# Kernel optimization log

Hardware: AMD Instinct MI355X
Metric: run time of the kernel (lower is better)

## Reference

```python
import jax, jax.numpy as jnp
import numpy as np

N, E = 50000, 800000
C, NT, ET, H, D = 128, 8, 16, 64, 4
TOTAL_IN = 2 * C + 2 * NT + ET  # 288
EPS = 1e-5


def setup_inputs() -> dict:
    key = jax.random.key(0)
    ks = jax.random.split(key, 10)
    x = jax.random.normal(ks[0], (N, C), dtype=jnp.float32)
    edge_index = jax.random.randint(ks[1], (2, E), 0, N, dtype=jnp.int64)
    edge_types = jax.random.randint(ks[2], (E,), 0, ET, dtype=jnp.int64)
    node_types = jax.random.randint(ks[3], (N,), 0, NT, dtype=jnp.int64)
    ln_w = jnp.ones((TOTAL_IN,), dtype=jnp.float32)
    ln_b = jnp.zeros((TOTAL_IN,), dtype=jnp.float32)
    W1 = jax.random.normal(ks[4], (TOTAL_IN, H), dtype=jnp.float32) * 0.05
    b1 = jnp.zeros((H,), dtype=jnp.float32)
    W2 = jax.random.normal(ks[5], (H, D * D), dtype=jnp.float32) * 0.05
    b2 = jnp.zeros((D * D,), dtype=jnp.float32)
    return {"x": x, "edge_index": edge_index, "edge_types": edge_types,
            "node_types": node_types, "ln_w": ln_w, "ln_b": ln_b,
            "W1": W1, "b1": b1, "W2": W2, "b2": b2}


def reference(x, edge_index, edge_types, node_types, ln_w, ln_b, W1, b1, W2, b2):
    row, col = edge_index[0], edge_index[1]
    # edge gathers of node features and one-hot type encodings
    nt_oh = jax.nn.one_hot(node_types, NT, dtype=x.dtype)   # [N, NT]
    et_oh = jax.nn.one_hot(edge_types, ET, dtype=x.dtype)   # [E, ET]
    h = jnp.concatenate([x[row], x[col], nt_oh[row], nt_oh[col], et_oh], axis=-1)  # [E, 288]
    # LayerNorm
    mu = jnp.mean(h, axis=-1, keepdims=True)
    var = jnp.mean(jnp.square(h - mu), axis=-1, keepdims=True)
    h = (h - mu) * jax.lax.rsqrt(var + EPS) * ln_w + ln_b
    # small MLP
    h = jax.nn.relu(h @ W1 + b1) @ W2 + b2          # [E, D*D]
    h = h.reshape(-1, D, D)
    att = jax.nn.softmax(h, axis=-1)                 # row-stochastic per edge
    return jnp.eye(D, dtype=h.dtype)[None] - att     # [E, D, D]
```

## Files before the change

kernel.cpp:

```cpp
#include <hip/hip_runtime.h>
#include <hip/hip_bf16.h>

#define NN 50000
#define NE 800000
#define C 128
#define HH 64
#define TIN 288
#define LN_EPS 1e-5f

typedef __attribute__((ext_vector_type(8))) short bf16x8;
typedef __attribute__((ext_vector_type(4))) float f32x4;

#define ETT_OFF 512
#define B1F_OFF 2560
#define B2F_OFF 35328
#define OHU_OFF 37376
#define OHV_OFF 38400
#define SQ_OFF 39424
#define U_OFF 439424
#define V_OFF 6839424

__device__ __forceinline__ short f2bf(float f) {
    __hip_bfloat16 h = __float2bfloat16(f);
    return __builtin_bit_cast(short, h);
}
__device__ __forceinline__ float bf2f(short s) {
    unsigned int u = ((unsigned int)(unsigned short)s) << 16;
    return __builtin_bit_cast(float, u);
}

__global__ void prep_weights(const float* __restrict__ ln_w,
                             const float* __restrict__ ln_b,
                             const float* __restrict__ W1,
                             const float* __restrict__ b1,
                             const float* __restrict__ W2,
                             float* __restrict__ ws) {
    int gid = blockIdx.x * 256 + threadIdx.x;
    if (blockIdx.x == 0 && threadIdx.x < 64) {
        int l = threadIdx.x;
        float s = 0.f, c = 0.f;
        for (int k = 0; k < TIN; ++k) {
            float w = W1[k * HH + l];
            s += ln_w[k] * w;
            c += ln_b[k] * w;
        }
        ws[l] = s;
        ws[64 + l] = c + b1[l];
    }
    short* B1 = (short*)((char*)ws + B1F_OFF);
    for (int idx = gid; idx < 16384; idx += 8192) {
        int j = idx & 7, l = (idx >> 3) & 63, cc = (idx >> 9) & 3, kt = idx >> 11;
        int g = l >> 4, m = l & 15;
        int k = 32 * kt + 8 * g + j, n = 16 * cc + m;
        B1[idx] = f2bf(ln_w[k] * W1[k * HH + n]);
    }
    short* B2 = (short*)((char*)ws + B2F_OFF);
    for (int idx = gid; idx < 1024; idx += 8192) {
        int j = idx & 7, l = (idx >> 3) & 63, kt = idx >> 9;
        int g = l >> 4, m = l & 15;
        int k = 32 * kt + 8 * g + j;
        B2[idx] = f2bf(W2[k * 16 + m]);
    }
    short* ohu = (short*)((char*)ws + OHU_OFF);
    short* ohv = (short*)((char*)ws + OHV_OFF);
    for (int idx = gid; idx < 512; idx += 8192) {
        int t = idx >> 6, j = idx & 63;
        ohu[idx] = f2bf(ln_w[256 + t] * W1[(256 + t) * HH + j]);
        ohv[idx] = f2bf(ln_w[264 + t] * W1[(264 + t) * HH + j]);
    }
    short* ett = (short*)((char*)ws + ETT_OFF);
    for (int idx = gid; idx < 1024; idx += 8192) {
        int et = idx >> 6, j = idx & 63;
        int unit = (j >> 3) ^ (et & 7);
        ett[et * 64 + unit * 8 + (j & 7)] = f2bf(ln_w[272 + et] * W1[(272 + et) * HH + j]);
    }
}

__global__ __launch_bounds__(512) void node_uv(const float* __restrict__ x,
                                               const int* __restrict__ ntype,
                                               float* __restrict__ ws) {
    __shared__ __align__(16) short lds_n[16384 + 8 * 1024];
    int tid = threadIdx.x;
    {
        const float4* src = (const float4*)((const char*)ws + B1F_OFF);
        float4* dst = (float4*)lds_n;
        for (int i = tid; i < 2048; i += 512) dst[i] = src[i];
    }
    __syncthreads();

    int wave = tid >> 6, lane = tid & 63, m = lane & 15, g = lane >> 4;
    int tile = blockIdx.x * 128 + wave * 16;
    int n = tile + m;
    int nc = n < NN ? n : NN - 1;

    float sum = 0.f, sq = 0.f;
    bf16x8 a[4];
#pragma unroll
    for (int kt = 0; kt < 4; ++kt) {
        const float* p = x + (size_t)nc * C + kt * 32 + g * 8;
        float4 p0 = *(const float4*)p;
        float4 p1 = *(const float4*)(p + 4);
        float vv[8] = {p0.x, p0.y, p0.z, p0.w, p1.x, p1.y, p1.z, p1.w};
#pragma unroll
        for (int j = 0; j < 8; ++j) {
            sum += vv[j];
            sq = fmaf(vv[j], vv[j], sq);
            a[kt][j] = f2bf(vv[j]);
        }
    }
    sum += __shfl_xor(sum, 16); sum += __shfl_xor(sum, 32);
    sq  += __shfl_xor(sq, 16);  sq  += __shfl_xor(sq, 32);
    if (g == 0 && n < NN)
        ((float2*)((char*)ws + SQ_OFF))[n] = make_float2(sum, sq);

    f32x4 au[4], av[4];
#pragma unroll
    for (int cc = 0; cc < 4; ++cc) { au[cc] = (f32x4){0,0,0,0}; av[cc] = (f32x4){0,0,0,0}; }
#pragma unroll
    for (int kt = 0; kt < 4; ++kt) {
        const bf16x8* Bu = (const bf16x8*)(lds_n + (kt * 4) * 512);
        const bf16x8* Bv = (const bf16x8*)(lds_n + ((kt + 4) * 4) * 512);
#pragma unroll
        for (int cc = 0; cc < 4; ++cc) {
            au[cc] = __builtin_amdgcn_mfma_f32_16x16x32_bf16(a[kt], Bu[cc * 64 + lane], au[cc], 0, 0, 0);
            av[cc] = __builtin_amdgcn_mfma_f32_16x16x32_bf16(a[kt], Bv[cc * 64 + lane], av[cc], 0, 0, 0);
        }
    }

    int ntv[4];
#pragma unroll
    for (int i = 0; i < 4; ++i) {
        int nn = tile + 4 * g + i;
        ntv[i] = ntype[nn < NN ? nn : NN - 1];
    }
    const unsigned short* ohu = (const unsigned short*)((const char*)ws + OHU_OFF);
    const unsigned short* ohv = (const unsigned short*)((const char*)ws + OHV_OFF);
    unsigned short* uT = (unsigned short*)((char*)ws + U_OFF);
    unsigned short* vT = (unsigned short*)((char*)ws + V_OFF);
    short* tb = lds_n + 16384 + wave * 1024;
    int nst = tile + m;

#pragma unroll
    for (int cc = 0; cc < 4; ++cc)
#pragma unroll
        for (int i = 0; i < 4; ++i) {
            float val = au[cc][i] + bf2f((short)ohu[ntv[i] * 64 + 16 * cc + m]);
            int r16 = 4 * g + i;
            tb[(r16 * 64 + 16 * cc + m) ^ ((r16 & 7) << 3)] = f2bf(val);
        }
    if (nst < NN) {
#pragma unroll
        for (int s2 = 0; s2 < 2; ++s2) {
            int idx = (m * 64 + 16 * g + 8 * s2) ^ ((m & 7) << 3);
            *(bf16x8*)(uT + (size_t)nst * 64 + 16 * g + 8 * s2) = *(const bf16x8*)(tb + idx);
        }
    }
#pragma unroll
    for (int cc = 0; cc < 4; ++cc)
#pragma unroll
        for (int i = 0; i < 4; ++i) {
            float val = av[cc][i] + bf2f((short)ohv[ntv[i] * 64 + 16 * cc + m]);
            int r16 = 4 * g + i;
            tb[(r16 * 64 + 16 * cc + m) ^ ((r16 & 7) << 3)] = f2bf(val);
        }
    if (nst < NN) {
#pragma unroll
        for (int s2 = 0; s2 < 2; ++s2) {
            int idx = (m * 64 + 16 * g + 8 * s2) ^ ((m & 7) << 3);
            *(bf16x8*)(vT + (size_t)nst * 64 + 16 * g + 8 * s2) = *(const bf16x8*)(tb + idx);
        }
    }
}

__global__ __launch_bounds__(512) void edge_kernel(
    const int* __restrict__ ei,
    const int* __restrict__ etype,
    const float* __restrict__ ws,
    const float* __restrict__ b2,
    float* __restrict__ out) {
    __shared__ __align__(16) short lds_e[2048];
    int tid = threadIdx.x;
    if (tid < 128)
        ((float4*)lds_e)[tid] = *(const float4*)((const char*)ws + B2F_OFF + tid * 16);
    else if (tid < 256)
        ((float4*)lds_e)[tid] = *(const float4*)((const char*)ws + ETT_OFF + (tid - 128) * 16);
    __syncthreads();

    int wave = tid >> 6, lane = tid & 63, m = lane & 15, g = lane >> 4;
    int tile = blockIdx.x * 128 + wave * 16;
    int e = tile + m;

    int row = ei[e];
    int col = ei[NE + e];
    int et = etype[e];

    const float2* SQ = (const float2*)((const char*)ws + SQ_OFF);
    float2 sqr = SQ[row], sqc = SQ[col];
    const unsigned short* uT = (const unsigned short*)((const char*)ws + U_OFF);
    const unsigned short* vT = (const unsigned short*)((const char*)ws + V_OFF);
    bf16x8 U0 = *(const bf16x8*)(uT + (size_t)row * 64 + 8 * g);
    bf16x8 U1 = *(const bf16x8*)(uT + (size_t)row * 64 + 32 + 8 * g);
    bf16x8 V0 = *(const bf16x8*)(vT + (size_t)col * 64 + 8 * g);
    bf16x8 V1 = *(const bf16x8*)(vT + (size_t)col * 64 + 32 + 8 * g);
    const short* ett = lds_e + 1024;
    bf16x8 T0 = *(const bf16x8*)(ett + et * 64 + ((g ^ (et & 7)) << 3));
    bf16x8 T1 = *(const bf16x8*)(ett + et * 64 + (((4 + g) ^ (et & 7)) << 3));

    float mu = (sqr.x + sqc.x + 3.0f) * (1.0f / TIN);
    float var = (sqr.y + sqc.y + 3.0f) * (1.0f / TIN) - mu * mu;
    float rstd = rsqrtf(var + LN_EPS);

    const float* sst = ws;
    const float* cct = ws + 64;
    bf16x8 af0, af1;
    {
        f32x4 sA = *(const f32x4*)(sst + 8 * g);
        f32x4 sB = *(const f32x4*)(sst + 8 * g + 4);
        f32x4 cA = *(const f32x4*)(cct + 8 * g);
        f32x4 cB = *(const f32x4*)(cct + 8 * g + 4);
#pragma unroll
        for (int j = 0; j < 8; ++j) {
            float t = bf2f(U0[j]) + bf2f(V0[j]) + bf2f(T0[j]);
            float sv = (j < 4) ? sA[j] : sB[j - 4];
            float cv = (j < 4) ? cA[j] : cB[j - 4];
            float h = rstd * (t - mu * sv) + cv;
            af0[j] = f2bf(fmaxf(h, 0.f));
        }
    }
    {
        f32x4 sA = *(const f32x4*)(sst + 32 + 8 * g);
        f32x4 sB = *(const f32x4*)(sst + 32 + 8 * g + 4);
        f32x4 cA = *(const f32x4*)(cct + 32 + 8 * g);
        f32x4 cB = *(const f32x4*)(cct + 32 + 8 * g + 4);
#pragma unroll
        for (int j = 0; j < 8; ++j) {
            float t = bf2f(U1[j]) + bf2f(V1[j]) + bf2f(T1[j]);
            float sv = (j < 4) ? sA[j] : sB[j - 4];
            float cv = (j < 4) ? cA[j] : cB[j - 4];
            float h = rstd * (t - mu * sv) + cv;
            af1[j] = f2bf(fmaxf(h, 0.f));
        }
    }

    const bf16x8* B2f = (const bf16x8*)lds_e;
    f32x4 o = {0.f, 0.f, 0.f, 0.f};
    o = __builtin_amdgcn_mfma_f32_16x16x32_bf16(af0, B2f[lane], o, 0, 0, 0);
    o = __builtin_amdgcn_mfma_f32_16x16x32_bf16(af1, B2f[64 + lane], o, 0, 0, 0);

    float b2v = b2[m];
    int r4 = m >> 2, c4 = m & 3;
    float diag = (c4 == r4) ? 1.0f : 0.0f;
#pragma unroll
    for (int i = 0; i < 4; ++i) {
        float v = o[i] + b2v;
        float mx = fmaxf(v, __shfl_xor(v, 1));
        mx = fmaxf(mx, __shfl_xor(mx, 2));
        float ev = __expf(v - mx);
        float sd = ev + __shfl_xor(ev, 1);
        sd += __shfl_xor(sd, 2);
        out[(size_t)(tile + 4 * g + i) * 16 + m] = diag - ev / sd;
    }
}

extern "C" void kernel_launch(void* const* d_in, const int* in_sizes, int n_in,
                              void* d_out, int out_size, void* d_ws, size_t ws_size,
                              hipStream_t stream) {
    const float* x     = (const float*)d_in[0];
    const int*   ei    = (const int*)d_in[1];
    const int*   etype = (const int*)d_in[2];
    const int*   ntype = (const int*)d_in[3];
    const float* ln_w  = (const float*)d_in[4];
    const float* ln_b  = (const float*)d_in[5];
    const float* W1    = (const float*)d_in[6];
    const float* b1    = (const float*)d_in[7];
    const float* W2    = (const float*)d_in[8];
    const float* b2    = (const float*)d_in[9];
    float* out = (float*)d_out;
    float* ws  = (float*)d_ws;

    prep_weights<<<32, 256, 0, stream>>>(ln_w, ln_b, W1, b1, W2, ws);
    node_uv<<<(NN + 127) / 128, 512, 0, stream>>>(x, ntype, ws);
    edge_kernel<<<NE / 128, 512, 0, stream>>>(ei, etype, ws, b2, out);
}
```

Measured before the change: 78.42 us.

## Process two edge tiles per wave with transposed MFMA and in-lane softmax

Each wave now handles 32 edges instead of 16: index loads are issued before the LDS barrier and all gathers for both tiles are issued up front to increase memory-level parallelism. The MFMA operands are swapped so each lane holds the four entries of one softmax row, which removes the cross-lane shuffles and allows float4 stores. LayerNorm arithmetic is folded into fused multiply-adds, and the grid is halved with a launch-bounds occupancy hint. Register pressure rises, which could limit occupancy.

```diff
diff --git a/kernel.cpp b/kernel.cpp
--- a/kernel.cpp
+++ b/kernel.cpp
@@ -172,7 +172,7 @@
     }
 }
 
-__global__ __launch_bounds__(512) void edge_kernel(
+__global__ __launch_bounds__(512, 3) void edge_kernel(
     const int* __restrict__ ei,
     const int* __restrict__ etype,
     const float* __restrict__ ws,
@@ -180,85 +180,95 @@
     float* __restrict__ out) {
     __shared__ __align__(16) short lds_e[2048];
     int tid = threadIdx.x;
+    int wave = tid >> 6, lane = tid & 63, m = lane & 15, g = lane >> 4;
+    int base = blockIdx.x * 256 + wave * 32;
+    int e0 = base + m, e1 = base + 16 + m;
+
+    int row0 = ei[e0], col0 = ei[NE + e0], et0 = etype[e0];
+    int row1 = ei[e1], col1 = ei[NE + e1], et1 = etype[e1];
+
     if (tid < 128)
         ((float4*)lds_e)[tid] = *(const float4*)((const char*)ws + B2F_OFF + tid * 16);
     else if (tid < 256)
         ((float4*)lds_e)[tid] = *(const float4*)((const char*)ws + ETT_OFF + (tid - 128) * 16);
     __syncthreads();
 
-    int wave = tid >> 6, lane = tid & 63, m = lane & 15, g = lane >> 4;
-    int tile = blockIdx.x * 128 + wave * 16;
-    int e = tile + m;
-
-    int row = ei[e];
-    int col = ei[NE + e];
-    int et = etype[e];
-
     const float2* SQ = (const float2*)((const char*)ws + SQ_OFF);
-    float2 sqr = SQ[row], sqc = SQ[col];
+    float2 sqr0 = SQ[row0], sqc0 = SQ[col0];
+    float2 sqr1 = SQ[row1], sqc1 = SQ[col1];
     const unsigned short* uT = (const unsigned short*)((const char*)ws + U_OFF);
     const unsigned short* vT = (const unsigned short*)((const char*)ws + V_OFF);
-    bf16x8 U0 = *(const bf16x8*)(uT + (size_t)row * 64 + 8 * g);
-    bf16x8 U1 = *(const bf16x8*)(uT + (size_t)row * 64 + 32 + 8 * g);
-    bf16x8 V0 = *(const bf16x8*)(vT + (size_t)col * 64 + 8 * g);
-    bf16x8 V1 = *(const bf16x8*)(vT + (size_t)col * 64 + 32 + 8 * g);
+    bf16x8 U00 = *(const bf16x8*)(uT + (size_t)row0 * 64 + 8 * g);
+    bf16x8 U01 = *(const bf16x8*)(uT + (size_t)row0 * 64 + 32 + 8 * g);
+    bf16x8 V00 = *(const bf16x8*)(vT + (size_t)col0 * 64 + 8 * g);
+    bf16x8 V01 = *(const bf16x8*)(vT + (size_t)col0 * 64 + 32 + 8 * g);
+    bf16x8 U10 = *(const bf16x8*)(uT + (size_t)row1 * 64 + 8 * g);
+    bf16x8 U11 = *(const bf16x8*)(uT + (size_t)row1 * 64 + 32 + 8 * g);
+    bf16x8 V10 = *(const bf16x8*)(vT + (size_t)col1 * 64 + 8 * g);
+    bf16x8 V11 = *(const bf16x8*)(vT + (size_t)col1 * 64 + 32 + 8 * g);
+    f32x4 s00 = *(const f32x4*)(ws + 8 * g);
+    f32x4 s01 = *(const f32x4*)(ws + 8 * g + 4);
+    f32x4 s10 = *(const f32x4*)(ws + 32 + 8 * g);
+    f32x4 s11 = *(const f32x4*)(ws + 36 + 8 * g);
+    f32x4 c00 = *(const f32x4*)(ws + 64 + 8 * g);
+    f32x4 c01 = *(const f32x4*)(ws + 64 + 8 * g + 4);
+    f32x4 c10 = *(const f32x4*)(ws + 96 + 8 * g);
+    f32x4 c11 = *(const f32x4*)(ws + 100 + 8 * g);
+    float4 b2q = *(const float4*)(b2 + 4 * g);
+    asm volatile("" ::: "memory");
+
+    const bf16x8* W2A = (const bf16x8*)lds_e;
+    bf16x8 w0 = W2A[lane], w1 = W2A[64 + lane];
     const short* ett = lds_e + 1024;
-    bf16x8 T0 = *(const bf16x8*)(ett + et * 64 + ((g ^ (et & 7)) << 3));
-    bf16x8 T1 = *(const bf16x8*)(ett + et * 64 + (((4 + g) ^ (et & 7)) << 3));
-
-    float mu = (sqr.x + sqc.x + 3.0f) * (1.0f / TIN);
-    float var = (sqr.y + sqc.y + 3.0f) * (1.0f / TIN) - mu * mu;
-    float rstd = rsqrtf(var + LN_EPS);
-
-    const float* sst = ws;
-    const float* cct = ws + 64;
-    bf16x8 af0, af1;
-    {
-        f32x4 sA = *(const f32x4*)(sst + 8 * g);
-        f32x4 sB = *(const f32x4*)(sst + 8 * g + 4);
-        f32x4 cA = *(const f32x4*)(cct + 8 * g);
-        f32x4 cB = *(const f32x4*)(cct + 8 * g + 4);
-#pragma unroll
-        for (int j = 0; j < 8; ++j) {
-            float t = bf2f(U0[j]) + bf2f(V0[j]) + bf2f(T0[j]);
-            float sv = (j < 4) ? sA[j] : sB[j - 4];
-            float cv = (j < 4) ? cA[j] : cB[j - 4];
-            float h = rstd * (t - mu * sv) + cv;
+
+#pragma unroll
+    for (int t = 0; t < 2; ++t) {
+        int et = t ? et1 : et0;
+        float2 sqr = t ? sqr1 : sqr0, sqc = t ? sqc1 : sqc0;
+        bf16x8 U0 = t ? U10 : U00, U1 = t ? U11 : U01;
+        bf16x8 V0 = t ? V10 : V00, V1 = t ? V11 : V01;
+
+        bf16x8 T0 = *(const bf16x8*)(ett + et * 64 + ((g ^ (et & 7)) << 3));
+        bf16x8 T1 = *(const bf16x8*)(ett + et * 64 + (((4 + g) ^ (et & 7)) << 3));
+
+        float mu = (sqr.x + sqc.x + 3.0f) * (1.0f / TIN);
+        float var = (sqr.y + sqc.y + 3.0f) * (1.0f / TIN) - mu * mu;
+        float rstd = rsqrtf(var + LN_EPS);
+        float rm = rstd * mu;
+
+        bf16x8 af0, af1;
+#pragma unroll
+        for (int j = 0; j < 4; ++j) {
+            float tt = bf2f(U0[j]) + bf2f(V0[j]) + bf2f(T0[j]);
+            float h = fmaf(rstd, tt, fmaf(-rm, s00[j], c00[j]));
             af0[j] = f2bf(fmaxf(h, 0.f));
-        }
-    }
-    {
-        f32x4 sA = *(const f32x4*)(sst + 32 + 8 * g);
-        f32x4 sB = *(const f32x4*)(sst + 32 + 8 * g + 4);
-        f32x4 cA = *(const f32x4*)(cct + 32 + 8 * g);
-        f32x4 cB = *(const f32x4*)(cct + 32 + 8 * g + 4);
-#pragma unroll
-        for (int j = 0; j < 8; ++j) {
-            float t = bf2f(U1[j]) + bf2f(V1[j]) + bf2f(T1[j]);
-            float sv = (j < 4) ? sA[j] : sB[j - 4];
-            float cv = (j < 4) ? cA[j] : cB[j - 4];
-            float h = rstd * (t - mu * sv) + cv;
-            af1[j] = f2bf(fmaxf(h, 0.f));
-        }
-    }
-
-    const bf16x8* B2f = (const bf16x8*)lds_e;
-    f32x4 o = {0.f, 0.f, 0.f, 0.f};
-    o = __builtin_amdgcn_mfma_f32_16x16x32_bf16(af0, B2f[lane], o, 0, 0, 0);
-    o = __builtin_amdgcn_mfma_f32_16x16x32_bf16(af1, B2f[64 + lane], o, 0, 0, 0);
-
-    float b2v = b2[m];
-    int r4 = m >> 2, c4 = m & 3;
-    float diag = (c4 == r4) ? 1.0f : 0.0f;
-#pragma unroll
-    for (int i = 0; i < 4; ++i) {
-        float v = o[i] + b2v;
-        float mx = fmaxf(v, __shfl_xor(v, 1));
-        mx = fmaxf(mx, __shfl_xor(mx, 2));
-        float ev = __expf(v - mx);
-        float sd = ev + __shfl_xor(ev, 1);
-        sd += __shfl_xor(sd, 2);
-        out[(size_t)(tile + 4 * g + i) * 16 + m] = diag - ev / sd;
+            float tt2 = bf2f(U0[j + 4]) + bf2f(V0[j + 4]) + bf2f(T0[j + 4]);
+            float h2 = fmaf(rstd, tt2, fmaf(-rm, s01[j], c01[j]));
+            af0[j + 4] = f2bf(fmaxf(h2, 0.f));
+            float tt3 = bf2f(U1[j]) + bf2f(V1[j]) + bf2f(T1[j]);
+            float h3 = fmaf(rstd, tt3, fmaf(-rm, s10[j], c10[j]));
+            af1[j] = f2bf(fmaxf(h3, 0.f));
+            float tt4 = bf2f(U1[j + 4]) + bf2f(V1[j + 4]) + bf2f(T1[j + 4]);
+            float h4 = fmaf(rstd, tt4, fmaf(-rm, s11[j], c11[j]));
+            af1[j + 4] = f2bf(fmaxf(h4, 0.f));
+        }
+
+        f32x4 o = {0.f, 0.f, 0.f, 0.f};
+        o = __builtin_amdgcn_mfma_f32_16x16x32_bf16(w0, af0, o, 0, 0, 0);
+        o = __builtin_amdgcn_mfma_f32_16x16x32_bf16(w1, af1, o, 0, 0, 0);
+
+        float v0 = o[0] + b2q.x, v1 = o[1] + b2q.y;
+        float v2 = o[2] + b2q.z, v3 = o[3] + b2q.w;
+        float mx = fmaxf(fmaxf(v0, v1), fmaxf(v2, v3));
+        float x0 = __expf(v0 - mx), x1 = __expf(v1 - mx);
+        float x2 = __expf(v2 - mx), x3 = __expf(v3 - mx);
+        float inv = 1.0f / (x0 + x1 + x2 + x3);
+        float4 res;
+        res.x = (g == 0 ? 1.0f : 0.0f) - x0 * inv;
+        res.y = (g == 1 ? 1.0f : 0.0f) - x1 * inv;
+        res.z = (g == 2 ? 1.0f : 0.0f) - x2 * inv;
+        res.w = (g == 3 ? 1.0f : 0.0f) - x3 * inv;
+        *(float4*)(out + (size_t)(base + 16 * t + m) * 16 + 4 * g) = res;
     }
 }
 
@@ -280,5 +290,5 @@
 
     prep_weights<<<32, 256, 0, stream>>>(ln_w, ln_b, W1, b1, W2, ws);
     node_uv<<<(NN + 127) / 128, 512, 0, stream>>>(x, ntype, ws);
-    edge_kernel<<<NE / 128, 512, 0, stream>>>(ei, etype, ws, b2, out);
-}
+    edge_kernel<<<NE / 256, 512, 0, stream>>>(ei, etype, ws, b2, out);
+}
```

New measurement: 78.52 us. About the same (+0.1%).
